# Optimization experiments

Hardware: AMD Instinct MI355X
Metric: run time of the kernel (lower is better)

Reference implementation:

```python
import jax, jax.numpy as jnp
import numpy as np

B, D, H, FPL, L, LOG2_T = 65536, 768, 512, 4, 16, 19
T = 2 ** LOG2_T
BASE_RES, FINEST_RES = 16, 512
PRIMES = jnp.array([1, 2654435761, 805459861], dtype=jnp.uint32)


def setup_inputs() -> dict:
    key = jax.random.key(0)
    ks = jax.random.split(key, 8)
    t = jax.random.uniform(ks[0], (B,), dtype=jnp.float32)
    x = jax.random.normal(ks[1], (B, D), dtype=jnp.float32)
    cond = jax.random.uniform(ks[2], (B, 2), dtype=jnp.float32)
    # one embedding table per level, Instant-NGP init U(-1e-4, 1e-4)
    tables = jax.random.uniform(ks[3], (L, T, FPL), dtype=jnp.float32,
                                minval=-1e-4, maxval=1e-4)
    in_dim = D + L * FPL  # 832

    def lin(k, fan_in, fan_out):
        return jax.random.normal(k, (fan_in, fan_out), dtype=jnp.float32) / np.sqrt(fan_in).astype(np.float32)

    W0, b0 = lin(ks[4], in_dim, H), jnp.zeros((H,), jnp.float32)
    W1, b1 = lin(ks[5], H, H), jnp.zeros((H,), jnp.float32)
    W2, b2 = lin(ks[6], H, H), jnp.zeros((H,), jnp.float32)
    W3, b3 = lin(ks[7], H, D), jnp.zeros((D,), jnp.float32)
    return dict(t=t, x=x, cond=cond, tables=tables,
                W0=W0, b0=b0, W1=W1, b1=b1, W2=W2, b2=b2, W3=W3, b3=b3)


def hash_encode(coords, tables):
    """coords: [B,3] in [0,1]; tables: [L,T,F] -> [B, L*F]."""
    Ln, Tn, Fn = tables.shape
    growth = np.exp((np.log(FINEST_RES) - np.log(BASE_RES)) / (Ln - 1))
    scales = jnp.asarray(np.floor(BASE_RES * growth ** np.arange(Ln)),
                         dtype=coords.dtype)                      # [L]
    xf = coords[:, None, :] * scales[None, :, None]               # [B,L,3]
    xl = jnp.floor(xf)
    w = xf - xl                                                   # [B,L,3] trilinear frac
    xi = xl.astype(jnp.uint32)
    # 8 cube-corner offsets
    offs = jnp.asarray(np.stack(np.meshgrid([0, 1], [0, 1], [0, 1],
                                            indexing='ij'), -1).reshape(8, 3),
                       dtype=jnp.uint32)                          # [8,3]
    corners = xi[:, :, None, :] + offs[None, None]                # [B,L,8,3]
    h = corners * PRIMES                                          # uint32 wraparound hash
    idx = (h[..., 0] ^ h[..., 1] ^ h[..., 2]) & jnp.uint32(Tn - 1)  # [B,L,8]
    feats = tables[jnp.arange(Ln)[None, :, None], idx]            # [B,L,8,F] gather
    offs_f = offs.astype(coords.dtype)
    wc = jnp.prod(jnp.where(offs_f[None, None] == 1,
                            w[:, :, None, :], 1 - w[:, :, None, :]), axis=-1)  # [B,L,8]
    out = jnp.einsum('blc,blcf->blf', wc, feats)                  # [B,L,F]
    return out.reshape(out.shape[0], Ln * Fn)


def reference(t, x, cond, tables, W0, b0, W1, b1, W2, b2, W3, b3):
    tcol = t[:, None] if t.ndim == 1 else t
    params3 = jnp.concatenate([cond, tcol], axis=-1)   # [B,3]
    enc = hash_encode(params3, tables)                  # [B,64]
    h = jnp.concatenate([x, enc], axis=-1)              # [B,832]
    h = jax.nn.silu(h @ W0 + b0)
    h = jax.nn.silu(h @ W1 + b1)
    h = jax.nn.silu(h @ W2 + b2)
    return h @ W3 + b3                                  # [B,768]
```

## Files before the change

kernel.cpp:

```cpp
#include <hip/hip_runtime.h>
#include <hip/hip_bf16.h>
#include <math.h>


#define T_SIZE 524288
#define T_MASK (T_SIZE - 1)

typedef _Float16 f16;
typedef _Float16 f16x8 __attribute__((ext_vector_type(8)));
typedef _Float16 f16x4 __attribute__((ext_vector_type(4)));
typedef float f32x4 __attribute__((ext_vector_type(4)));

struct Scales { float s[16]; };

__global__ void wfrag(const float* __restrict__ W, f16* __restrict__ Wf, int K, int N) {
  int tid = blockIdx.x * 256 + threadIdx.x;
  int lane = tid & 63, frag = tid >> 6;
  int KS = K >> 5;
  int nblk = frag / KS, ks = frag - nblk * KS;
  if (nblk * 16 >= N) return;
  int n = nblk * 16 + (lane & 15);
  int kb = ks * 32 + (lane >> 4) * 8;
  f16x8 v;
#pragma unroll
  for (int j = 0; j < 8; ++j) v[j] = (f16)W[(size_t)(kb + j) * N + n];
  *(f16x8*)(Wf + (size_t)frag * 512 + lane * 8) = v;
}

__device__ __forceinline__ float silu_f(float v) {
  return v * __builtin_amdgcn_rcpf(1.f + __expf(-v));
}

template<int NF, int KSTEPS>
__device__ __forceinline__ void kloop_dp(
    const f16* __restrict__ actS, const f16* __restrict__ Wf, int fragRow0,
    int l16, int lhi, int lane, f32x4 (&acc)[4][4]) {
#pragma unroll
  for (int mi = 0; mi < 4; ++mi)
#pragma unroll
    for (int ni = 0; ni < NF; ++ni) acc[mi][ni] = (f32x4){0.f, 0.f, 0.f, 0.f};

  f16x8 bfU[NF], bfV[NF];
  const f16* wbase = Wf + ((size_t)fragRow0 * KSTEPS) * 512 + lane * 8;
#pragma unroll
  for (int ni = 0; ni < NF; ++ni)
    bfU[ni] = *(const f16x8*)(wbase + (size_t)(ni * KSTEPS + 0) * 512);
#pragma unroll
  for (int ni = 0; ni < NF; ++ni)
    bfV[ni] = *(const f16x8*)(wbase + (size_t)(ni * KSTEPS + 1) * 512);

#pragma unroll 1
  for (int ks = 0; ks < KSTEPS; ks += 2) {
    f16x8 af[4];
#pragma unroll
    for (int mi = 0; mi < 4; ++mi) {
      int r = mi * 16 + l16;
      af[mi] = *(const f16x8*)(actS + r * 512 + ((ks * 32 + lhi * 8) ^ ((r & 7) << 3)));
    }
#pragma unroll
    for (int mi = 0; mi < 4; ++mi)
#pragma unroll
      for (int ni = 0; ni < NF; ++ni)
        acc[mi][ni] = __builtin_amdgcn_mfma_f32_16x16x32_f16(bfU[ni], af[mi], acc[mi][ni], 0, 0, 0);
    if (ks + 2 < KSTEPS) {
#pragma unroll
      for (int ni = 0; ni < NF; ++ni)
        bfU[ni] = *(const f16x8*)(wbase + (size_t)(ni * KSTEPS + ks + 2) * 512);
    }
#pragma unroll
    for (int mi = 0; mi < 4; ++mi) {
      int r = mi * 16 + l16;
      af[mi] = *(const f16x8*)(actS + r * 512 + (((ks + 1) * 32 + lhi * 8) ^ ((r & 7) << 3)));
    }
#pragma unroll
    for (int mi = 0; mi < 4; ++mi)
#pragma unroll
      for (int ni = 0; ni < NF; ++ni)
        acc[mi][ni] = __builtin_amdgcn_mfma_f32_16x16x32_f16(bfV[ni], af[mi], acc[mi][ni], 0, 0, 0);
    if (ks + 3 < KSTEPS) {
#pragma unroll
      for (int ni = 0; ni < NF; ++ni)
        bfV[ni] = *(const f16x8*)(wbase + (size_t)(ni * KSTEPS + ks + 3) * 512);
    }
  }
}

__global__ __launch_bounds__(512, 4) void fused_mlp(
    const float* __restrict__ x, const float* __restrict__ t,
    const float* __restrict__ cond, const float* __restrict__ tables,
    const f16* __restrict__ Wf0, const f16* __restrict__ Wf1,
    const f16* __restrict__ Wf2, const f16* __restrict__ Wf3,
    const float* __restrict__ b0, const float* __restrict__ b1,
    const float* __restrict__ b2, const float* __restrict__ b3,
    float* __restrict__ out, Scales scl) {
  __shared__ f16 act[64 * 512];
  __shared__ f16 stg[2 * 64 * 40];

  const int tid = threadIdx.x;
  const int wave = tid >> 6, lane = tid & 63;
  const int l16 = lane & 15, lhi = lane >> 4;
  const int rowBase = blockIdx.x * 64;
  const int sr = tid >> 3, sc = tid & 7;

  f16x4 er_a, er_b;
  {
    int row = rowBase + sr;
    float c0 = cond[2 * row], c1 = cond[2 * row + 1], c2 = t[row];
#pragma unroll
    for (int h = 0; h < 2; ++h) {
      int l = sc + h * 8;
      float s = scl.s[l];
      float xf0 = c0 * s, xf1 = c1 * s, xf2 = c2 * s;
      float xl0 = floorf(xf0), xl1 = floorf(xf1), xl2 = floorf(xf2);
      float w0 = xf0 - xl0, w1 = xf1 - xl1, w2 = xf2 - xl2;
      unsigned xi0 = (unsigned)xl0, xi1 = (unsigned)xl1, xi2 = (unsigned)xl2;
      const float4* tl = (const float4*)tables + (size_t)l * T_SIZE;
      float a0 = 0.f, a1 = 0.f, a2 = 0.f, a3 = 0.f;
#pragma unroll
      for (int c = 0; c < 8; ++c) {
        unsigned ax = (c >> 2) & 1u, ay = (c >> 1) & 1u, az = c & 1u;
        unsigned hh = (xi0 + ax) ^ ((xi1 + ay) * 2654435761u) ^ ((xi2 + az) * 805459861u);
        float4 f = tl[hh & T_MASK];
        float wcw = (ax ? w0 : 1.f - w0) * (ay ? w1 : 1.f - w1) * (az ? w2 : 1.f - w2);
        a0 += wcw * f.x; a1 += wcw * f.y; a2 += wcw * f.z; a3 += wcw * f.w;
      }
      f16x4 er = { (f16)a0, (f16)a1, (f16)a2, (f16)a3 };
      if (h == 0) er_a = er; else er_b = er;
    }
  }

  f32x4 acc[4][4];

#pragma unroll
  for (int mi = 0; mi < 4; ++mi)
#pragma unroll
    for (int ni = 0; ni < 4; ++ni) acc[mi][ni] = (f32x4){0.f, 0.f, 0.f, 0.f};

  {
    float4 a = *(const float4*)(x + (size_t)(rowBase + sr) * 768 + sc * 4);
    f16x4 v = { (f16)a.x, (f16)a.y, (f16)a.z, (f16)a.w };
    *(f16x4*)(stg + sr * 40 + sc * 4) = v;
  }
  f16x8 bfA[4], bfB[4];
#pragma unroll
  for (int ni = 0; ni < 4; ++ni)
    bfA[ni] = *(const f16x8*)(Wf0 + ((size_t)(wave * 4 + ni) * 26) * 512 + lane * 8);
  __syncthreads();

#pragma unroll 1
  for (int ks = 0; ks < 26; ++ks) {
    const int nxt = ks + 1;
    f16x4 nv;
    if (nxt < 24) {
      float4 a = *(const float4*)(x + (size_t)(rowBase + sr) * 768 + nxt * 32 + sc * 4);
      nv = (f16x4){ (f16)a.x, (f16)a.y, (f16)a.z, (f16)a.w };
    } else {
      nv = (nxt == 24) ? er_a : er_b;
    }
    if (nxt < 26) {
#pragma unroll
      for (int ni = 0; ni < 4; ++ni)
        bfB[ni] = *(const f16x8*)(Wf0 + ((size_t)(wave * 4 + ni) * 26 + nxt) * 512 + lane * 8);
    }
    const f16* rb = stg + (ks & 1) * 2560;
#pragma unroll
    for (int mi = 0; mi < 4; ++mi) {
      f16x8 af = *(const f16x8*)(rb + (mi * 16 + l16) * 40 + lhi * 8);
#pragma unroll
      for (int ni = 0; ni < 4; ++ni)
        acc[mi][ni] = __builtin_amdgcn_mfma_f32_16x16x32_f16(bfA[ni], af, acc[mi][ni], 0, 0, 0);
    }
    if (nxt < 26) {
      *(f16x4*)(stg + (nxt & 1) * 2560 + sr * 40 + sc * 4) = nv;
#pragma unroll
      for (int ni = 0; ni < 4; ++ni) bfA[ni] = bfB[ni];
    }
    __syncthreads();
  }

  auto epi_act = [&](const float* __restrict__ bias) {
    __syncthreads();
#pragma unroll
    for (int mi = 0; mi < 4; ++mi) {
      const int row = mi * 16 + l16;
#pragma unroll
      for (int ni = 0; ni < 4; ++ni) {
        const int col = wave * 64 + ni * 16 + lhi * 4;
        float4 bv = *(const float4*)(bias + col);
        f16x4 o;
        o[0] = (f16)silu_f(acc[mi][ni][0] + bv.x);
        o[1] = (f16)silu_f(acc[mi][ni][1] + bv.y);
        o[2] = (f16)silu_f(acc[mi][ni][2] + bv.z);
        o[3] = (f16)silu_f(acc[mi][ni][3] + bv.w);
        *(f16x4*)(act + row * 512 + (col ^ ((row & 7) << 3))) = o;
      }
    }
    __syncthreads();
  };
  epi_act(b0);

  kloop_dp<4, 16>(act, Wf1, wave * 4, l16, lhi, lane, acc); epi_act(b1);
  kloop_dp<4, 16>(act, Wf2, wave * 4, l16, lhi, lane, acc); epi_act(b2);

  kloop_dp<4, 16>(act, Wf3, wave * 4, l16, lhi, lane, acc);
#pragma unroll
  for (int mi = 0; mi < 4; ++mi) {
    const size_t row = (size_t)(rowBase + mi * 16 + l16);
#pragma unroll
    for (int ni = 0; ni < 4; ++ni) {
      const int col = wave * 64 + ni * 16 + lhi * 4;
      float4 bv = *(const float4*)(b3 + col);
      float4 o = { acc[mi][ni][0] + bv.x, acc[mi][ni][1] + bv.y,
                   acc[mi][ni][2] + bv.z, acc[mi][ni][3] + bv.w };
      *(float4*)(out + row * 768 + col) = o;
    }
  }

  kloop_dp<2, 16>(act, Wf3, 32 + wave * 2, l16, lhi, lane, acc);
#pragma unroll
  for (int mi = 0; mi < 4; ++mi) {
    const size_t row = (size_t)(rowBase + mi * 16 + l16);
#pragma unroll
    for (int ni = 0; ni < 2; ++ni) {
      const int col = 512 + wave * 32 + ni * 16 + lhi * 4;
      float4 bv = *(const float4*)(b3 + col);
      float4 o = { acc[mi][ni][0] + bv.x, acc[mi][ni][1] + bv.y,
                   acc[mi][ni][2] + bv.z, acc[mi][ni][3] + bv.w };
      *(float4*)(out + row * 768 + col) = o;
    }
  }
}

extern "C" void kernel_launch(void* const* d_in, const int* in_sizes, int n_in,
                              void* d_out, int out_size, void* d_ws, size_t ws_size,
                              hipStream_t stream) {
  const float* t    = (const float*)d_in[0];
  const float* x    = (const float*)d_in[1];
  const float* cond = (const float*)d_in[2];
  const float* tab  = (const float*)d_in[3];
  const float* W0   = (const float*)d_in[4];
  const float* b0   = (const float*)d_in[5];
  const float* W1   = (const float*)d_in[6];
  const float* b1   = (const float*)d_in[7];
  const float* W2   = (const float*)d_in[8];
  const float* b2   = (const float*)d_in[9];
  const float* W3   = (const float*)d_in[10];
  const float* b3   = (const float*)d_in[11];
  float* out = (float*)d_out;
  (void)in_sizes; (void)n_in; (void)out_size; (void)ws_size;

  char* ws = (char*)d_ws;
  f16* Wf0 = (f16*)(ws + 0);
  f16* Wf1 = (f16*)(ws + 851968);
  f16* Wf2 = (f16*)(ws + 1376256);
  f16* Wf3 = (f16*)(ws + 1900544);

  wfrag<<<dim3(208), 256, 0, stream>>>(W0, Wf0, 832, 512);
  wfrag<<<dim3(128), 256, 0, stream>>>(W1, Wf1, 512, 512);
  wfrag<<<dim3(128), 256, 0, stream>>>(W2, Wf2, 512, 512);
  wfrag<<<dim3(192), 256, 0, stream>>>(W3, Wf3, 512, 768);

  Scales sc;
  {
    double growth = exp((log(512.0) - log(16.0)) / 15.0);
    for (int l = 0; l < 16; ++l) sc.s[l] = (float)floor(16.0 * pow(growth, (double)l));
  }

  fused_mlp<<<dim3(1024), 512, 0, stream>>>(x, t, cond, tab, Wf0, Wf1, Wf2, Wf3,
                                            b0, b1, b2, b3, out, sc);
}
```

Before: 301.5 us.

## Load x directly into MFMA fragments, stage encoding in LDS, drop per-step barriers

Layer 0 now reads x straight from global memory into registers in MFMA fragment layout and converts it to f16 there, instead of staging each 32-column slice through a double-buffered LDS tile with a __syncthreads every step. The hash encoding is written once to a swizzled LDS buffer and consumed in the final two k-steps, and the weight fragments are double-buffered as in the later layers. Output stores become nontemporal and launch bounds drop from 4 to 2 blocks per CU, giving the compiler more registers. The cost is that each lane issues uncoalesced 32-byte x loads whose latency is not hidden by LDS staging, and residency may fall.

```diff
diff --git a/kernel.cpp b/kernel.cpp
--- a/kernel.cpp
+++ b/kernel.cpp
@@ -31,6 +31,11 @@
   return v * __builtin_amdgcn_rcpf(1.f + __expf(-v));
 }
 
+__device__ __forceinline__ f16x8 cvt8(f32x4 a, f32x4 b) {
+  return (f16x8){ (f16)a.x, (f16)a.y, (f16)a.z, (f16)a.w,
+                  (f16)b.x, (f16)b.y, (f16)b.z, (f16)b.w };
+}
+
 template<int NF, int KSTEPS>
 __device__ __forceinline__ void kloop_dp(
     const f16* __restrict__ actS, const f16* __restrict__ Wf, int fragRow0,
@@ -85,16 +90,16 @@
   }
 }
 
-__global__ __launch_bounds__(512, 4) void fused_mlp(
+__global__ __launch_bounds__(512, 2) void fused_mlp(
     const float* __restrict__ x, const float* __restrict__ t,
     const float* __restrict__ cond, const float* __restrict__ tables,
     const f16* __restrict__ Wf0, const f16* __restrict__ Wf1,
     const f16* __restrict__ Wf2, const f16* __restrict__ Wf3,
     const float* __restrict__ b0, const float* __restrict__ b1,
     const float* __restrict__ b2, const float* __restrict__ b3,
-    float* __restrict__ out, Scales scl) {
+    float* __restrict__ outp, Scales scl) {
   __shared__ f16 act[64 * 512];
-  __shared__ f16 stg[2 * 64 * 40];
+  __shared__ f16 encs[64 * 64];
 
   const int tid = threadIdx.x;
   const int wave = tid >> 6, lane = tid & 63;
@@ -102,7 +107,6 @@
   const int rowBase = blockIdx.x * 64;
   const int sr = tid >> 3, sc = tid & 7;
 
-  f16x4 er_a, er_b;
   {
     int row = rowBase + sr;
     float c0 = cond[2 * row], c1 = cond[2 * row + 1], c2 = t[row];
@@ -125,57 +129,77 @@
         a0 += wcw * f.x; a1 += wcw * f.y; a2 += wcw * f.z; a3 += wcw * f.w;
       }
       f16x4 er = { (f16)a0, (f16)a1, (f16)a2, (f16)a3 };
-      if (h == 0) er_a = er; else er_b = er;
+      int col = (h * 32 + sc * 4) ^ ((sr & 7) << 3);
+      *(f16x4*)(encs + sr * 64 + col) = er;
     }
   }
 
   f32x4 acc[4][4];
-
 #pragma unroll
   for (int mi = 0; mi < 4; ++mi)
 #pragma unroll
     for (int ni = 0; ni < 4; ++ni) acc[mi][ni] = (f32x4){0.f, 0.f, 0.f, 0.f};
 
   {
-    float4 a = *(const float4*)(x + (size_t)(rowBase + sr) * 768 + sc * 4);
-    f16x4 v = { (f16)a.x, (f16)a.y, (f16)a.z, (f16)a.w };
-    *(f16x4*)(stg + sr * 40 + sc * 4) = v;
-  }
-  f16x8 bfA[4], bfB[4];
-#pragma unroll
-  for (int ni = 0; ni < 4; ++ni)
-    bfA[ni] = *(const f16x8*)(Wf0 + ((size_t)(wave * 4 + ni) * 26) * 512 + lane * 8);
-  __syncthreads();
+    const float* xb[4];
+#pragma unroll
+    for (int mi = 0; mi < 4; ++mi)
+      xb[mi] = x + (size_t)(rowBase + mi * 16 + l16) * 768 + lhi * 8;
+
+    f16x8 bfU[4], bfV[4];
+    const f16* wbase = Wf0 + lane * 8;
+#pragma unroll
+    for (int ni = 0; ni < 4; ++ni)
+      bfU[ni] = *(const f16x8*)(wbase + (size_t)((wave * 4 + ni) * 26 + 0) * 512);
+#pragma unroll
+    for (int ni = 0; ni < 4; ++ni)
+      bfV[ni] = *(const f16x8*)(wbase + (size_t)((wave * 4 + ni) * 26 + 1) * 512);
+
+    __syncthreads();
 
 #pragma unroll 1
-  for (int ks = 0; ks < 26; ++ks) {
-    const int nxt = ks + 1;
-    f16x4 nv;
-    if (nxt < 24) {
-      float4 a = *(const float4*)(x + (size_t)(rowBase + sr) * 768 + nxt * 32 + sc * 4);
-      nv = (f16x4){ (f16)a.x, (f16)a.y, (f16)a.z, (f16)a.w };
-    } else {
-      nv = (nxt == 24) ? er_a : er_b;
-    }
-    if (nxt < 26) {
-#pragma unroll
-      for (int ni = 0; ni < 4; ++ni)
-        bfB[ni] = *(const f16x8*)(Wf0 + ((size_t)(wave * 4 + ni) * 26 + nxt) * 512 + lane * 8);
-    }
-    const f16* rb = stg + (ks & 1) * 2560;
-#pragma unroll
-    for (int mi = 0; mi < 4; ++mi) {
-      f16x8 af = *(const f16x8*)(rb + (mi * 16 + l16) * 40 + lhi * 8);
-#pragma unroll
-      for (int ni = 0; ni < 4; ++ni)
-        acc[mi][ni] = __builtin_amdgcn_mfma_f32_16x16x32_f16(bfA[ni], af, acc[mi][ni], 0, 0, 0);
-    }
-    if (nxt < 26) {
-      *(f16x4*)(stg + (nxt & 1) * 2560 + sr * 40 + sc * 4) = nv;
-#pragma unroll
-      for (int ni = 0; ni < 4; ++ni) bfA[ni] = bfB[ni];
-    }
-    __syncthreads();
+    for (int ks = 0; ks < 24; ks += 2) {
+#pragma unroll
+      for (int mi = 0; mi < 4; ++mi) {
+        f32x4 a = *(const f32x4*)(xb[mi] + ks * 32);
+        f32x4 b = *(const f32x4*)(xb[mi] + ks * 32 + 4);
+        f16x8 af = cvt8(a, b);
+#pragma unroll
+        for (int ni = 0; ni < 4; ++ni)
+          acc[mi][ni] = __builtin_amdgcn_mfma_f32_16x16x32_f16(bfU[ni], af, acc[mi][ni], 0, 0, 0);
+      }
+#pragma unroll
+      for (int ni = 0; ni < 4; ++ni)
+        bfU[ni] = *(const f16x8*)(wbase + (size_t)((wave * 4 + ni) * 26 + ks + 2) * 512);
+#pragma unroll
+      for (int mi = 0; mi < 4; ++mi) {
+        f32x4 a = *(const f32x4*)(xb[mi] + (ks + 1) * 32);
+        f32x4 b = *(const f32x4*)(xb[mi] + (ks + 1) * 32 + 4);
+        f16x8 af = cvt8(a, b);
+#pragma unroll
+        for (int ni = 0; ni < 4; ++ni)
+          acc[mi][ni] = __builtin_amdgcn_mfma_f32_16x16x32_f16(bfV[ni], af, acc[mi][ni], 0, 0, 0);
+      }
+#pragma unroll
+      for (int ni = 0; ni < 4; ++ni)
+        bfV[ni] = *(const f16x8*)(wbase + (size_t)((wave * 4 + ni) * 26 + ks + 3) * 512);
+    }
+#pragma unroll
+    for (int mi = 0; mi < 4; ++mi) {
+      int r = mi * 16 + l16;
+      f16x8 af = *(const f16x8*)(encs + r * 64 + ((lhi * 8) ^ ((r & 7) << 3)));
+#pragma unroll
+      for (int ni = 0; ni < 4; ++ni)
+        acc[mi][ni] = __builtin_amdgcn_mfma_f32_16x16x32_f16(bfU[ni], af, acc[mi][ni], 0, 0, 0);
+    }
+#pragma unroll
+    for (int mi = 0; mi < 4; ++mi) {
+      int r = mi * 16 + l16;
+      f16x8 af = *(const f16x8*)(encs + r * 64 + ((32 + lhi * 8) ^ ((r & 7) << 3)));
+#pragma unroll
+      for (int ni = 0; ni < 4; ++ni)
+        acc[mi][ni] = __builtin_amdgcn_mfma_f32_16x16x32_f16(bfV[ni], af, acc[mi][ni], 0, 0, 0);
+    }
   }
 
   auto epi_act = [&](const float* __restrict__ bias) {
@@ -210,9 +234,9 @@
     for (int ni = 0; ni < 4; ++ni) {
       const int col = wave * 64 + ni * 16 + lhi * 4;
       float4 bv = *(const float4*)(b3 + col);
-      float4 o = { acc[mi][ni][0] + bv.x, acc[mi][ni][1] + bv.y,
-                   acc[mi][ni][2] + bv.z, acc[mi][ni][3] + bv.w };
-      *(float4*)(out + row * 768 + col) = o;
+      f32x4 o = { acc[mi][ni][0] + bv.x, acc[mi][ni][1] + bv.y,
+                  acc[mi][ni][2] + bv.z, acc[mi][ni][3] + bv.w };
+      __builtin_nontemporal_store(o, (f32x4*)(outp + row * 768 + col));
     }
   }
 
@@ -224,9 +248,9 @@
     for (int ni = 0; ni < 2; ++ni) {
       const int col = 512 + wave * 32 + ni * 16 + lhi * 4;
       float4 bv = *(const float4*)(b3 + col);
-      float4 o = { acc[mi][ni][0] + bv.x, acc[mi][ni][1] + bv.y,
-                   acc[mi][ni][2] + bv.z, acc[mi][ni][3] + bv.w };
-      *(float4*)(out + row * 768 + col) = o;
+      f32x4 o = { acc[mi][ni][0] + bv.x, acc[mi][ni][1] + bv.y,
+                  acc[mi][ni][2] + bv.z, acc[mi][ni][3] + bv.w };
+      __builtin_nontemporal_store(o, (f32x4*)(outp + row * 768 + col));
     }
   }
 }
```

Measured after the change: 443.7 us. 1.47x slower.

## Restructure layer-0 K loop to 64-wide steps with staging aliased into act LDS

Applied to the files above, without the earlier changes.

The first-layer K loop now processes two 32-wide K slices per iteration, which halves the iteration count and the number of block barriers. Weight fragments are loaded at the top of each iteration instead of being double-buffered in registers. The x staging buffer now lives inside the existing act shared array, cutting total LDS per block and possibly raising occupancy. x loads and output stores become nontemporal 8-wide accesses. In exchange, weight-load latency is no longer hidden by prefetch.

```diff
diff --git a/kernel.cpp b/kernel.cpp
--- a/kernel.cpp
+++ b/kernel.cpp
@@ -31,6 +31,11 @@
   return v * __builtin_amdgcn_rcpf(1.f + __expf(-v));
 }
 
+__device__ __forceinline__ f16x8 cvt8(f32x4 a, f32x4 b) {
+  return (f16x8){ (f16)a.x, (f16)a.y, (f16)a.z, (f16)a.w,
+                  (f16)b.x, (f16)b.y, (f16)b.z, (f16)b.w };
+}
+
 template<int NF, int KSTEPS>
 __device__ __forceinline__ void kloop_dp(
     const f16* __restrict__ actS, const f16* __restrict__ Wf, int fragRow0,
@@ -92,23 +97,25 @@
     const f16* __restrict__ Wf2, const f16* __restrict__ Wf3,
     const float* __restrict__ b0, const float* __restrict__ b1,
     const float* __restrict__ b2, const float* __restrict__ b3,
-    float* __restrict__ out, Scales scl) {
+    float* __restrict__ outp, Scales scl) {
   __shared__ f16 act[64 * 512];
-  __shared__ f16 stg[2 * 64 * 40];
+  f16* stg = act;
+#define STG(p, kk) (stg + (p) * 5120 + (kk) * 2560)
 
   const int tid = threadIdx.x;
   const int wave = tid >> 6, lane = tid & 63;
   const int l16 = lane & 15, lhi = lane >> 4;
   const int rowBase = blockIdx.x * 64;
-  const int sr = tid >> 3, sc = tid & 7;
-
-  f16x4 er_a, er_b;
+  const int sr = tid >> 3, c8 = tid & 7;
+  const int skk = c8 >> 2, sco = (c8 & 3) * 8;
+
+  f16x8 er;
   {
     int row = rowBase + sr;
     float c0 = cond[2 * row], c1 = cond[2 * row + 1], c2 = t[row];
 #pragma unroll
-    for (int h = 0; h < 2; ++h) {
-      int l = sc + h * 8;
+    for (int d = 0; d < 2; ++d) {
+      int l = c8 * 2 + d;
       float s = scl.s[l];
       float xf0 = c0 * s, xf1 = c1 * s, xf2 = c2 * s;
       float xl0 = floorf(xf0), xl1 = floorf(xf1), xl2 = floorf(xf2);
@@ -124,58 +131,63 @@
         float wcw = (ax ? w0 : 1.f - w0) * (ay ? w1 : 1.f - w1) * (az ? w2 : 1.f - w2);
         a0 += wcw * f.x; a1 += wcw * f.y; a2 += wcw * f.z; a3 += wcw * f.w;
       }
-      f16x4 er = { (f16)a0, (f16)a1, (f16)a2, (f16)a3 };
-      if (h == 0) er_a = er; else er_b = er;
+      er[d * 4 + 0] = (f16)a0; er[d * 4 + 1] = (f16)a1;
+      er[d * 4 + 2] = (f16)a2; er[d * 4 + 3] = (f16)a3;
     }
   }
 
   f32x4 acc[4][4];
-
 #pragma unroll
   for (int mi = 0; mi < 4; ++mi)
 #pragma unroll
     for (int ni = 0; ni < 4; ++ni) acc[mi][ni] = (f32x4){0.f, 0.f, 0.f, 0.f};
 
   {
-    float4 a = *(const float4*)(x + (size_t)(rowBase + sr) * 768 + sc * 4);
-    f16x4 v = { (f16)a.x, (f16)a.y, (f16)a.z, (f16)a.w };
-    *(f16x4*)(stg + sr * 40 + sc * 4) = v;
-  }
-  f16x8 bfA[4], bfB[4];
-#pragma unroll
-  for (int ni = 0; ni < 4; ++ni)
-    bfA[ni] = *(const f16x8*)(Wf0 + ((size_t)(wave * 4 + ni) * 26) * 512 + lane * 8);
-  __syncthreads();
+    const float* xrow = x + (size_t)(rowBase + sr) * 768 + c8 * 8;
+    {
+      f32x4 a = __builtin_nontemporal_load((const f32x4*)(xrow));
+      f32x4 b = __builtin_nontemporal_load((const f32x4*)(xrow + 4));
+      *(f16x8*)(STG(0, skk) + sr * 40 + sco) = cvt8(a, b);
+    }
+    const f16* wb = Wf0 + lane * 8;
+    __syncthreads();
 
 #pragma unroll 1
-  for (int ks = 0; ks < 26; ++ks) {
-    const int nxt = ks + 1;
-    f16x4 nv;
-    if (nxt < 24) {
-      float4 a = *(const float4*)(x + (size_t)(rowBase + sr) * 768 + nxt * 32 + sc * 4);
-      nv = (f16x4){ (f16)a.x, (f16)a.y, (f16)a.z, (f16)a.w };
-    } else {
-      nv = (nxt == 24) ? er_a : er_b;
-    }
-    if (nxt < 26) {
-#pragma unroll
-      for (int ni = 0; ni < 4; ++ni)
-        bfB[ni] = *(const f16x8*)(Wf0 + ((size_t)(wave * 4 + ni) * 26 + nxt) * 512 + lane * 8);
-    }
-    const f16* rb = stg + (ks & 1) * 2560;
-#pragma unroll
-    for (int mi = 0; mi < 4; ++mi) {
-      f16x8 af = *(const f16x8*)(rb + (mi * 16 + l16) * 40 + lhi * 8);
-#pragma unroll
-      for (int ni = 0; ni < 4; ++ni)
-        acc[mi][ni] = __builtin_amdgcn_mfma_f32_16x16x32_f16(bfA[ni], af, acc[mi][ni], 0, 0, 0);
-    }
-    if (nxt < 26) {
-      *(f16x4*)(stg + (nxt & 1) * 2560 + sr * 40 + sc * 4) = nv;
-#pragma unroll
-      for (int ni = 0; ni < 4; ++ni) bfA[ni] = bfB[ni];
-    }
-    __syncthreads();
+    for (int ks = 0; ks < 13; ++ks) {
+      f16x8 bf[2][4];
+#pragma unroll
+      for (int kk = 0; kk < 2; ++kk)
+#pragma unroll
+        for (int ni = 0; ni < 4; ++ni)
+          bf[kk][ni] = *(const f16x8*)(wb + (size_t)((wave * 4 + ni) * 26 + 2 * ks + kk) * 512);
+
+      f16x8 nv;
+      const bool hasNext = ks < 12;
+      if (hasNext) {
+        if (ks + 1 < 12) {
+          f32x4 a = __builtin_nontemporal_load((const f32x4*)(xrow + (ks + 1) * 64));
+          f32x4 b = __builtin_nontemporal_load((const f32x4*)(xrow + (ks + 1) * 64 + 4));
+          nv = cvt8(a, b);
+        } else {
+          nv = er;
+        }
+      }
+
+      const f16* rb = stg + (ks & 1) * 5120;
+#pragma unroll
+      for (int kk = 0; kk < 2; ++kk)
+#pragma unroll
+        for (int mi = 0; mi < 4; ++mi) {
+          f16x8 af = *(const f16x8*)(rb + kk * 2560 + (mi * 16 + l16) * 40 + lhi * 8);
+#pragma unroll
+          for (int ni = 0; ni < 4; ++ni)
+            acc[mi][ni] = __builtin_amdgcn_mfma_f32_16x16x32_f16(bf[kk][ni], af, acc[mi][ni], 0, 0, 0);
+        }
+
+      if (hasNext)
+        *(f16x8*)(STG((ks + 1) & 1, skk) + sr * 40 + sco) = nv;
+      __syncthreads();
+    }
   }
 
   auto epi_act = [&](const float* __restrict__ bias) {
@@ -210,9 +222,9 @@
     for (int ni = 0; ni < 4; ++ni) {
       const int col = wave * 64 + ni * 16 + lhi * 4;
       float4 bv = *(const float4*)(b3 + col);
-      float4 o = { acc[mi][ni][0] + bv.x, acc[mi][ni][1] + bv.y,
-                   acc[mi][ni][2] + bv.z, acc[mi][ni][3] + bv.w };
-      *(float4*)(out + row * 768 + col) = o;
+      f32x4 o = { acc[mi][ni][0] + bv.x, acc[mi][ni][1] + bv.y,
+                  acc[mi][ni][2] + bv.z, acc[mi][ni][3] + bv.w };
+      __builtin_nontemporal_store(o, (f32x4*)(outp + row * 768 + col));
     }
   }
 
@@ -224,11 +236,12 @@
     for (int ni = 0; ni < 2; ++ni) {
       const int col = 512 + wave * 32 + ni * 16 + lhi * 4;
       float4 bv = *(const float4*)(b3 + col);
-      float4 o = { acc[mi][ni][0] + bv.x, acc[mi][ni][1] + bv.y,
-                   acc[mi][ni][2] + bv.z, acc[mi][ni][3] + bv.w };
-      *(float4*)(out + row * 768 + col) = o;
-    }
-  }
+      f32x4 o = { acc[mi][ni][0] + bv.x, acc[mi][ni][1] + bv.y,
+                  acc[mi][ni][2] + bv.z, acc[mi][ni][3] + bv.w };
+      __builtin_nontemporal_store(o, (f32x4*)(outp + row * 768 + col));
+    }
+  }
+#undef STG
 }
 
 extern "C" void kernel_launch(void* const* d_in, const int* in_sizes, int n_in,
```

Result: faster. 289.7 us (-3.9%).
